# Optimization experiments

Measured on AMD Instinct MI355X. Metric: run time of the kernel, lower is better.

## Reference

```python
import jax, jax.numpy as jnp
import numpy as np
from functools import partial

B, S, T = 32, 64, 64
VS, VT = 32000, 32000
E, H = 256, 512            # embed_dim, encoder hidden per direction
DH = 2 * H                 # decoder hidden (= encoder_hidden_dim)
A = 128                    # attention_dim


def _p(key, shape, scale=0.05):
    return scale * jax.random.normal(key, shape, dtype=jnp.float32)


def setup_inputs() -> dict:
    key = jax.random.key(0)
    ks = jax.random.split(key, 32)
    inp = {
        'src': jax.random.randint(ks[0], (B, S), 0, VS),
        'tgt_input': jax.random.randint(ks[1], (B, T), 0, VT),
        # encoder
        'enc_emb': _p(ks[2], (VS, E)),
        'enc_Wih_f': _p(ks[3], (4 * H, E)), 'enc_Whh_f': _p(ks[4], (4 * H, H)),
        'enc_bih_f': _p(ks[5], (4 * H,)),  'enc_bhh_f': _p(ks[6], (4 * H,)),
        'enc_Wih_b': _p(ks[7], (4 * H, E)), 'enc_Whh_b': _p(ks[8], (4 * H, H)),
        'enc_bih_b': _p(ks[9], (4 * H,)),  'enc_bhh_b': _p(ks[10], (4 * H,)),
        # decoder
        'dec_emb': _p(ks[11], (VT, E)),
        'Wd': _p(ks[12], (A, DH)), 'bd': _p(ks[13], (A,)),
        'We': _p(ks[14], (A, DH)), 'be': _p(ks[15], (A,)),
        'v_att': _p(ks[16], (A,)), 'bv': _p(ks[17], ()),
        'dec_Wih': _p(ks[18], (4 * DH, E + DH)), 'dec_Whh': _p(ks[19], (4 * DH, DH)),
        'dec_bih': _p(ks[20], (4 * DH,)), 'dec_bhh': _p(ks[21], (4 * DH,)),
        'Wo': _p(ks[22], (VT, DH + DH)), 'bo': _p(ks[23], (VT,)),
    }
    return inp


def _lstm_cell(x, h, c, Wih, Whh, b):
    g = x @ Wih.T + h @ Whh.T + b
    i, f, gg, o = jnp.split(g, 4, axis=-1)  # PyTorch gate order: i,f,g,o
    i, f, o = jax.nn.sigmoid(i), jax.nn.sigmoid(f), jax.nn.sigmoid(o)
    c_new = f * c + i * jnp.tanh(gg)
    h_new = o * jnp.tanh(c_new)
    return h_new, c_new


def _lstm_scan(xs, Wih, Whh, b, reverse):
    # xs: [S,B,E] -> outputs [S,B,H] aligned with input positions, final (h,c)
    h0 = jnp.zeros((xs.shape[1], Whh.shape[1]), xs.dtype)
    def step(carry, x):
        h, c = carry
        h, c = _lstm_cell(x, h, c, Wih, Whh, b)
        return (h, c), h
    (hT, cT), hs = jax.lax.scan(step, (h0, h0), xs, reverse=reverse)
    return hs, hT, cT


def _forward(src, tgt_input, enc_emb,
             enc_Wih_f, enc_Whh_f, enc_bih_f, enc_bhh_f,
             enc_Wih_b, enc_Whh_b, enc_bih_b, enc_bhh_b,
             dec_emb, Wd, bd, We, be, v_att, bv,
             dec_Wih, dec_Whh, dec_bih, dec_bhh, Wo, bo):
    # ---- Encoder: bidirectional single-layer LSTM ----
    emb = enc_emb[src]                              # [B,S,E]
    xs = emb.transpose(1, 0, 2)                     # [S,B,E]
    hs_f, hT_f, cT_f = _lstm_scan(xs, enc_Wih_f, enc_Whh_f, enc_bih_f + enc_bhh_f, False)
    hs_b, hT_b, cT_b = _lstm_scan(xs, enc_Wih_b, enc_Whh_b, enc_bih_b + enc_bhh_b, True)
    enc_out = jnp.concatenate([hs_f, hs_b], axis=-1).transpose(1, 0, 2)  # [B,S,2H]
    h = jnp.concatenate([hT_f, hT_b], axis=-1)      # [B,DH]
    c = jnp.concatenate([cT_f, cT_b], axis=-1)

    # ---- Decoder with Bahdanau attention (full teacher forcing) ----
    enc_proj = enc_out @ We.T + be                  # [B,S,A] precomputed
    dec_b = dec_bih + dec_bhh
    tgt_emb = dec_emb[tgt_input].transpose(1, 0, 2)  # [T,B,E]

    def dec_step(carry, emb_t):
        h, c = carry
        dproj = h @ Wd.T + bd                       # [B,A]
        energy = jnp.tanh(dproj[:, None, :] + enc_proj)  # [B,S,A]
        scores = energy @ v_att + bv                # [B,S]
        w = jax.nn.softmax(scores, axis=1)
        ctx = jnp.einsum('bs,bsh->bh', w, enc_out)  # [B,DH]
        x = jnp.concatenate([emb_t, ctx], axis=-1)  # [B,E+DH]
        h_new, c_new = _lstm_cell(x, h, c, dec_Wih, dec_Whh, dec_b)
        logits = jnp.concatenate([h_new, ctx], axis=-1) @ Wo.T + bo  # [B,VT]
        return (h_new, c_new), logits

    _, logits = jax.lax.scan(dec_step, (h, c), tgt_emb)  # [T,B,VT]
    return logits.transpose(1, 0, 2)                     # [B,T,VT]


def reference(src, tgt_input, enc_emb,
              enc_Wih_f, enc_Whh_f, enc_bih_f, enc_bhh_f,
              enc_Wih_b, enc_Whh_b, enc_bih_b, enc_bhh_b,
              dec_emb, Wd, bd, We, be, v_att, bv,
              dec_Wih, dec_Whh, dec_bih, dec_bhh, Wo, bo):
    return _forward(src, tgt_input, enc_emb,
                    enc_Wih_f, enc_Whh_f, enc_bih_f, enc_bhh_f,
                    enc_Wih_b, enc_Whh_b, enc_bih_b, enc_bhh_b,
                    dec_emb, Wd, bd, We, be, v_att, bv,
                    dec_Wih, dec_Whh, dec_bih, dec_bhh, Wo, bo)
```

## Files before the change

### kernel.cpp

```cpp
#include <hip/hip_runtime.h>


using u16 = unsigned short;
using u32 = unsigned int;
using u64 = unsigned long long;
using f32x4 = __attribute__((ext_vector_type(4))) float;
using s16x8 = __attribute__((ext_vector_type(8))) short;
using u16x4 = __attribute__((ext_vector_type(4))) unsigned short;

__device__ __forceinline__ float sigm_(float x) { return 1.0f / (1.0f + expf(-x)); }
__device__ __forceinline__ float tanh_(float x) {
    float e = __expf(fminf(2.0f * x, 30.0f));
    return (e - 1.0f) / (e + 1.0f);
}

__device__ __forceinline__ u16 f2bf(float x) {
    u32 u = __float_as_uint(x);
    u += 0x7fffu + ((u >> 16) & 1u);
    return (u16)(u >> 16);
}
__device__ __forceinline__ u32 pk2(float a, float b) {
    return (u32)f2bf(a) | ((u32)f2bf(b) << 16);
}
__device__ __forceinline__ float bf2f(u16 v) {
    return __uint_as_float((u32)v << 16);
}

__device__ __forceinline__ void ast32(u32* p, u32 v) {
    __hip_atomic_store(p, v, __ATOMIC_RELAXED, __HIP_MEMORY_SCOPE_AGENT);
}

#define MFMA __builtin_amdgcn_mfma_f32_16x16x32_bf16

#define GLL(g, l) __builtin_amdgcn_global_load_lds( \
    (__attribute__((address_space(1))) void*)(g),   \
    (__attribute__((address_space(3))) void*)(l), 16, 0, 0)

__device__ __forceinline__ void gbar(int* cnt, int target) {
    asm volatile("s_waitcnt vmcnt(0) lgkmcnt(0)" ::: "memory");
    __syncthreads();
    if (threadIdx.x == 0) {
        __hip_atomic_fetch_add(cnt, 1, __ATOMIC_RELAXED, __HIP_MEMORY_SCOPE_AGENT);
        while (__hip_atomic_load(cnt, __ATOMIC_RELAXED, __HIP_MEMORY_SCOPE_AGENT) < target)
            __builtin_amdgcn_s_sleep(1);
    }
    __syncthreads();
}

__global__ __launch_bounds__(256) void k_zero(float* __restrict__ p, int n) {
    int i = blockIdx.x * 256 + threadIdx.x;
    if (i < n) p[i] = 0.0f;
}

__global__ __launch_bounds__(256) void k_cast_bf16(const float* __restrict__ in,
                                                   u16* __restrict__ outp, int n8) {
    int idx = blockIdx.x * 256 + threadIdx.x;
    if (idx >= n8) return;
    const f32x4* p = (const f32x4*)in + (size_t)idx * 2;
    f32x4 a = p[0], c = p[1];
    u32* o = (u32*)(outp + (size_t)idx * 8);
    o[0] = pk2(a.x, a.y); o[1] = pk2(a.z, a.w);
    o[2] = pk2(c.x, c.y); o[3] = pk2(c.z, c.w);
}

__global__ __launch_bounds__(256) void k_embed_bf(const int* __restrict__ tok,
                                                  const float* __restrict__ emb,
                                                  u16* __restrict__ outp) {
    int idx = blockIdx.x * 256 + threadIdx.x;
    int r = idx >> 6, e4 = idx & 63;
    int outer = r >> 5, b = r & 31;
    int tk = tok[b * 64 + outer];
    f32x4 v = ((const f32x4*)emb)[(size_t)tk * 64 + e4];
    u32* o = (u32*)(outp + (size_t)r * 256 + (e4 << 2));
    o[0] = pk2(v.x, v.y); o[1] = pk2(v.z, v.w);
}

__global__ __launch_bounds__(256) void k_prep_perm(
    const float* __restrict__ src, u16* __restrict__ dst,
    int J, int K4, int srcStride, int srcOff, int total)
{
    int idx = blockIdx.x * 256 + threadIdx.x;
    if (idx >= total) return;
    int n = idx / K4, kq = (idx - n * K4) << 2;
    int orig = (n & 3) * J + (n >> 2);
    f32x4 v = *(const f32x4*)(src + (size_t)orig * srcStride + srcOff + kq);
    u32* o = (u32*)(dst + (size_t)n * (K4 << 2) + kq);
    o[0] = pk2(v.x, v.y); o[1] = pk2(v.z, v.w);
}

__global__ __launch_bounds__(256) void k_prep_ws(
    const float* __restrict__ W, u16* __restrict__ dst)
{
    int idx = blockIdx.x * 256 + threadIdx.x;
    int n = idx >> 8, kp = idx & 255, k0 = kp << 1;
    int orig = (n & 3) * 512 + (n >> 2);
    const float* s = W + (size_t)orig * 512 + k0;
    int g = n >> 5, r = n & 31;
    int byteoff = (k0 << 1) ^ ((r & 7) << 4);
    *(u32*)((char*)dst + (size_t)g * 32768 + r * 1024 + byteoff) = pk2(s[0], s[1]);
}

__global__ __launch_bounds__(256) void k_prep_w2s(
    const float* __restrict__ Whh, const float* __restrict__ Wih, u16* __restrict__ dst)
{
    int idx = blockIdx.x * 256 + threadIdx.x;
    int n = idx >> 10, kp = idx & 1023, k0 = kp << 1;
    int orig = (n & 3) * 1024 + (n >> 2);
    const float* s = (k0 < 1024) ? (Whh + (size_t)orig * 1024 + k0)
                                 : (Wih + (size_t)orig * 1280 + 256 + (k0 - 1024));
    int g = n >> 5, r = n & 31;
    int byteoff = (k0 << 1) ^ ((r & 7) << 4);
    *(u32*)((char*)dst + (size_t)g * 131072 + r * 4096 + byteoff) = pk2(s[0], s[1]);
}

__global__ __launch_bounds__(256) void k_gemm_bf(
    const u16* __restrict__ A, const u16* __restrict__ B, int K,
    const float* __restrict__ b1, const float* __restrict__ b2, int biasJ,
    float* __restrict__ C, int ldc, int nM, int nN, int remapOut, int swz)
{
    __shared__ __align__(16) u16 As[128 * 32];
    __shared__ __align__(16) u16 Bs[128 * 32];
    int w = blockIdx.x;
    if (swz) { int cpx = (nM * nN) >> 3; w = (w & 7) * cpx + (w >> 3); }
    int bm = (w % nM) * 128, bn = (w / nM) * 128;
    int tid = threadIdx.x, wave = tid >> 6, lane = tid & 63;
    int wm = wave & 1, wn = wave >> 1;
    f32x4 acc[4][4] = {};

    int rA = wave * 32 + (lane >> 2);
    int cb2 = (lane & 3) * 16;
    const char* gA = (const char*)A + ((size_t)(bm + rA) * K) * 2 + cb2;
    const char* gB = (const char*)B + ((size_t)(bn + rA) * K) * 2 + cb2;
    size_t rowskip = (size_t)16 * K * 2;
    char* lA = (char*)As + wave * 2048;
    char* lB = (char*)Bs + wave * 2048;
    const u16* rdA = As + (wm * 64 + (lane & 15)) * 32 + (lane >> 4) * 8;
    const u16* rdB = Bs + (wn * 64 + (lane & 15)) * 32 + (lane >> 4) * 8;

    for (int k0 = 0; k0 < K; k0 += 32) {
        size_t kb = (size_t)k0 * 2;
        GLL(gA + kb, lA); GLL(gA + kb + rowskip, lA + 1024);
        GLL(gB + kb, lB); GLL(gB + kb + rowskip, lB + 1024);
        __syncthreads();
        s16x8 af[4], bfv[4];
#pragma unroll
        for (int m2 = 0; m2 < 4; ++m2) af[m2] = *(const s16x8*)(rdA + m2 * 512);
#pragma unroll
        for (int n2 = 0; n2 < 4; ++n2) bfv[n2] = *(const s16x8*)(rdB + n2 * 512);
#pragma unroll
        for (int m2 = 0; m2 < 4; ++m2)
#pragma unroll
            for (int n2 = 0; n2 < 4; ++n2)
                acc[m2][n2] = MFMA(af[m2], bfv[n2], acc[m2][n2], 0, 0, 0);
        __syncthreads();
    }

    int rbase = bm + wm * 64 + ((lane >> 4) << 2);
    int cbase = bn + wn * 64 + (lane & 15);
#pragma unroll
    for (int n2 = 0; n2 < 4; ++n2) {
        int col = cbase + n2 * 16;
        int bcol = biasJ ? ((col & 3) * biasJ + (col >> 2)) : col;
        float bias = (b1 ? b1[bcol] : 0.0f) + (b2 ? b2[bcol] : 0.0f);
#pragma unroll
        for (int m2 = 0; m2 < 4; ++m2) {
            f32x4 v = acc[m2][n2];
#pragma unroll
            for (int jj = 0; jj < 4; ++jj) {
                int row = rbase + m2 * 16 + jj;
                int orow = remapOut ? ((row & 31) * 64 + (row >> 5)) : row;
                C[(size_t)orow * ldc + col] = v[jj] + bias;
            }
        }
    }
}

__global__ __launch_bounds__(256, 1) void k_enc_persist(
    const u16* __restrict__ Wsf, const u16* __restrict__ Wsb,
    const float* __restrict__ Gfp, const float* __restrict__ Gbp,
    u16* __restrict__ henc,
    float* __restrict__ cfb,
    u16* __restrict__ encbf,
    int* __restrict__ bar)
{
    __shared__ __align__(16) char smem[50176];
    int tid = threadIdx.x, lane = tid & 63, q = tid >> 6;
    int dir = blockIdx.x >> 6, g = blockIdx.x & 63;
    const char* wsrc = (const char*)(dir ? Wsb : Wsf) + (size_t)g * 32768;
#pragma unroll
    for (int it = 0; it < 8; ++it)
        GLL(wsrc + it * 4096 + tid * 16, smem + it * 4096 + tid * 16);
    __syncthreads();

    float* sacc = (float*)(smem + 32768);
    u16* hst = (u16*)(smem + 49664);
    const float* Gp = dir ? Gbp : Gfp;
    float* cB = cfb + dir * 16384;
    int lr = lane & 15, lk = (lane >> 4) << 3;
    int bb = tid & 31, jl = tid >> 5;
    int n0 = g * 32, j = g * 8 + jl;
    int bi = 0;

    for (int s = 0; s < 64; ++s) {
        const u16* hA = henc + (size_t)s * 32768 + dir * 16384;
        s16x8 afr[8];
#pragma unroll
        for (int it = 0; it < 4; ++it) {
            int ke = q * 128 + it * 32 + lk;
            afr[2 * it]     = *(const s16x8*)(hA + lr * 512 + ke);
            afr[2 * it + 1] = *(const s16x8*)(hA + (lr + 16) * 512 + ke);
        }
        f32x4 acc00 = {}, acc01 = {}, acc10 = {}, acc11 = {};
#pragma unroll
        for (int it = 0; it < 4; ++it) {
            int ke = q * 128 + it * 32 + lk;
            int kb = ke << 1;
            s16x8 b0 = *(const s16x8*)(smem + lr * 1024 + (kb ^ ((lr & 7) << 4)));
            int r1 = lr + 16;
            s16x8 b1 = *(const s16x8*)(smem + r1 * 1024 + (kb ^ ((r1 & 7) << 4)));
            acc00 = MFMA(afr[2 * it], b0, acc00, 0, 0, 0);
            acc01 = MFMA(afr[2 * it], b1, acc01, 0, 0, 0);
            acc10 = MFMA(afr[2 * it + 1], b0, acc10, 0, 0, 0);
            acc11 = MFMA(afr[2 * it + 1], b1, acc11, 0, 0, 0);
        }
        int rw = (lane >> 4) << 2;
#pragma unroll
        for (int rr = 0; rr < 4; ++rr) {
            sacc[q * 1056 + (rw + rr) * 33 + lr]        = acc00[rr];
            sacc[q * 1056 + (rw + rr) * 33 + 16 + lr]   = acc01[rr];
            sacc[q * 1056 + (16 + rw + rr) * 33 + lr]      = acc10[rr];
            sacc[q * 1056 + (16 + rw + rr) * 33 + 16 + lr] = acc11[rr];
        }
        __syncthreads();
        {
            int t = dir ? (63 - s) : s;
            int c4 = jl << 2;
            float gi = 0, gf = 0, gg = 0, go2 = 0;
#pragma unroll
            for (int q2 = 0; q2 < 4; ++q2) {
                const float* sp = sacc + q2 * 1056 + bb * 33 + c4;
                gi += sp[0]; gf += sp[1]; gg += sp[2]; go2 += sp[3];
            }
            f32x4 p4 = *(const f32x4*)(Gp + ((size_t)(t * 32 + bb)) * 2048 + n0 + c4);
            gi += p4.x; gf += p4.y; gg += p4.z; go2 += p4.w;
            float* cp = cB + bb * 512 + j;
            float cn = sigm_(gf) * cp[0] + sigm_(gi) * tanhf(gg);
            cp[0] = cn;
            float h = sigm_(go2) * tanhf(cn);
            u16 h16 = f2bf(h);
            encbf[((size_t)(bb * 64 + t)) * 1024 + dir * 512 + j] = h16;
            hst[bb * 8 + jl] = h16;
        }
        __syncthreads();
        if (tid < 128) {
            int bb2 = tid >> 2, p2 = tid & 3;
            u32 wv = (u32)hst[bb2 * 8 + 2 * p2] | ((u32)hst[bb2 * 8 + 2 * p2 + 1] << 16);
            ast32((u32*)(henc + (size_t)(s + 1) * 32768 + dir * 16384) + bb2 * 256 + g * 4 + p2, wv);
        }
        gbar(bar, (++bi) * 128);
    }
}

__global__ __launch_bounds__(256) void k_dec_init(
    const u16* __restrict__ henc, const float* __restrict__ cfb,
    u16* __restrict__ hcarr, float* __restrict__ cd)
{
    int idx = blockIdx.x * 256 + threadIdx.x;
    int b = idx >> 10, j = idx & 1023;
    int dir = (j >> 9), jj = j & 511;
    hcarr[b * 2048 + j] = henc[(size_t)64 * 32768 + dir * 16384 + b * 512 + jj];
    cd[b * 1024 + j] = cfb[dir * 16384 + b * 512 + jj];
}

__global__ __launch_bounds__(256, 1) void k_dec_persist(
    const u16* __restrict__ W2s, const u16* __restrict__ encbf,
    const float* __restrict__ Prep,
    const u16* __restrict__ Wd_bf, const float* __restrict__ bd,
    const float* __restrict__ eproj, const float* __restrict__ v_att,
    const float* __restrict__ bv,
    u16* __restrict__ hcarr, float* __restrict__ cd, u16* __restrict__ Abf,
    int* __restrict__ bar)
{
    __shared__ __align__(16) char smem[148480];
    int blk = blockIdx.x, tid = threadIdx.x, lane = tid & 63, q = tid >> 6;
    bool isgate = blk < 128;
    {
        const char* src = isgate ? ((const char*)W2s + (size_t)blk * 131072)
                                 : ((const char*)encbf + (size_t)(blk - 128) * 131072);
#pragma unroll
        for (int it = 0; it < 32; ++it)
            GLL(src + it * 4096 + tid * 16, smem + it * 4096 + tid * 16);
    }
    __syncthreads();

    float* sacc = (float*)(smem + 131072);
    u16* hst    = (u16*)(smem + 147968);
    float* hsh  = (float*)(smem + 131072);
    float* red  = (float*)(smem + 135168);
    float* dp   = (float*)(smem + 136192);
    float* sc   = (float*)(smem + 136704);

    int lr = lane & 15, lk = (lane >> 4) << 3;
    int bb = tid & 31, jl = tid >> 5;
    int n0 = blk * 32, j = blk * 8 + jl;
    int b = blk - 128;
    int bi = 0;

    for (int t = 0; t < 64; ++t) {
        const u16* hcT = hcarr + (size_t)t * 65536;
        f32x4 acc00 = {}, acc01 = {}, acc10 = {}, acc11 = {};
        f32x4 p4;
        if (isgate) {
            p4 = *(const f32x4*)(Prep + ((size_t)(t * 32 + bb)) * 4096 + n0 + (jl << 2));
            s16x8 afr[16];
#pragma unroll
            for (int it = 0; it < 8; ++it) {
                int ke = q * 256 + it * 32 + lk;
                afr[2 * it]     = *(const s16x8*)(hcT + lr * 2048 + ke);
                afr[2 * it + 1] = *(const s16x8*)(hcT + (lr + 16) * 2048 + ke);
            }
#pragma unroll
            for (int it = 0; it < 8; ++it) {
                int ke = q * 256 + it * 32 + lk;
                int kb = ke << 1;
                s16x8 b0 = *(const s16x8*)(smem + lr * 4096 + (kb ^ ((lr & 7) << 4)));
                int r1 = lr + 16;
                s16x8 b1 = *(const s16x8*)(smem + r1 * 4096 + (kb ^ ((r1 & 7) << 4)));
                acc00 = MFMA(afr[2 * it], b0, acc00, 0, 0, 0);
                acc01 = MFMA(afr[2 * it], b1, acc01, 0, 0, 0);
                acc10 = MFMA(afr[2 * it + 1], b0, acc10, 0, 0, 0);
                acc11 = MFMA(afr[2 * it + 1], b1, acc11, 0, 0, 0);
            }
        } else {
            {
                u16x4 hv = *(const u16x4*)(hcT + b * 2048 + (tid << 2));
                hsh[(tid << 2) + 0] = bf2f(hv.x);
                hsh[(tid << 2) + 1] = bf2f(hv.y);
                hsh[(tid << 2) + 2] = bf2f(hv.z);
                hsh[(tid << 2) + 3] = bf2f(hv.w);
            }
            __syncthreads();
            {
                int a = tid & 127, half = tid >> 7;
                const u16* wr = Wd_bf + ((size_t)a << 10) + (half << 9);
                const float* hh = hsh + (half << 9);
                float s0 = 0, s1 = 0, s2 = 0, s3 = 0;
#pragma unroll 4
                for (int k = 0; k < 512; k += 32) {
                    s16x8 w0 = *(const s16x8*)(wr + k);
                    s16x8 w1 = *(const s16x8*)(wr + k + 8);
                    s16x8 w2 = *(const s16x8*)(wr + k + 16);
                    s16x8 w3 = *(const s16x8*)(wr + k + 24);
#pragma unroll
                    for (int e = 0; e < 8; ++e) {
                        s0 += bf2f((u16)w0[e]) * hh[k + e];
                        s1 += bf2f((u16)w1[e]) * hh[k + 8 + e];
                        s2 += bf2f((u16)w2[e]) * hh[k + 16 + e];
                        s3 += bf2f((u16)w3[e]) * hh[k + 24 + e];
                    }
                }
                red[tid] = (s0 + s1) + (s2 + s3);
            }
            __syncthreads();
            if (tid < 128) dp[tid] = red[tid] + red[tid + 128] + bd[tid];
            __syncthreads();
            {
                int si = tid >> 2, qq = tid & 3;
                const float* ep = eproj + ((size_t)(b * 64 + si)) * 128 + qq * 32;
                float s = 0.0f;
#pragma unroll 8
                for (int a2 = 0; a2 < 32; ++a2)
                    s += v_att[qq * 32 + a2] * tanh_(dp[qq * 32 + a2] + ep[a2]);
                red[tid] = s;
            }
            __syncthreads();
            if (tid < 64) {
                float x = red[tid * 4] + red[tid * 4 + 1] + red[tid * 4 + 2] + red[tid * 4 + 3] + bv[0];
                float mx = x;
#pragma unroll
                for (int off = 32; off; off >>= 1) mx = fmaxf(mx, __shfl_xor(mx, off));
                float e = __expf(x - mx), ss = e;
#pragma unroll
                for (int off = 32; off; off >>= 1) ss += __shfl_xor(ss, off);
                sc[tid] = e / ss;
            }
            __syncthreads();
            {
                const u16* eL = (const u16*)smem;
                int c0i = tid << 2;
                float c0 = 0, c1 = 0, c2 = 0, c3 = 0;
                for (int s2 = 0; s2 < 64; ++s2) {
                    float wgt = sc[s2];
                    u16x4 rp = *(const u16x4*)(eL + s2 * 1024 + c0i);
                    c0 += wgt * bf2f(rp.x); c1 += wgt * bf2f(rp.y);
                    c2 += wgt * bf2f(rp.z); c3 += wgt * bf2f(rp.w);
                }
                u32 w0 = pk2(c0, c1), w1 = pk2(c2, c3);
                u32* hw = (u32*)hcT + b * 1024 + 512 + (tid << 1);
                ast32(hw, w0); ast32(hw + 1, w1);
                u32* aw = (u32*)(Abf + ((size_t)(t * 32 + b)) * 2048 + 1024 + c0i);
                aw[0] = w0; aw[1] = w1;
            }
        }
        gbar(bar, (++bi) * 160);
        if (isgate) {
            s16x8 afr[16];
#pragma unroll
            for (int it = 0; it < 8; ++it) {
                int ke = 1024 + q * 256 + it * 32 + lk;
                afr[2 * it]     = *(const s16x8*)(hcT + lr * 2048 + ke);
                afr[2 * it + 1] = *(const s16x8*)(hcT + (lr + 16) * 2048 + ke);
            }
#pragma unroll
            for (int it = 0; it < 8; ++it) {
                int ke = 1024 + q * 256 + it * 32 + lk;
                int kb = ke << 1;
                s16x8 b0 = *(const s16x8*)(smem + lr * 4096 + (kb ^ ((lr & 7) << 4)));
                int r1 = lr + 16;
                s16x8 b1 = *(const s16x8*)(smem + r1 * 4096 + (kb ^ ((r1 & 7) << 4)));
                acc00 = MFMA(afr[2 * it], b0, acc00, 0, 0, 0);
                acc01 = MFMA(afr[2 * it], b1, acc01, 0, 0, 0);
                acc10 = MFMA(afr[2 * it + 1], b0, acc10, 0, 0, 0);
                acc11 = MFMA(afr[2 * it + 1], b1, acc11, 0, 0, 0);
            }
            int rw = (lane >> 4) << 2;
#pragma unroll
            for (int rr = 0; rr < 4; ++rr) {
                sacc[q * 1056 + (rw + rr) * 33 + lr]        = acc00[rr];
                sacc[q * 1056 + (rw + rr) * 33 + 16 + lr]   = acc01[rr];
                sacc[q * 1056 + (16 + rw + rr) * 33 + lr]      = acc10[rr];
                sacc[q * 1056 + (16 + rw + rr) * 33 + 16 + lr] = acc11[rr];
            }
            __syncthreads();
            {
                int c4 = jl << 2;
                float gi = 0, gf = 0, gg = 0, go2 = 0;
#pragma unroll
                for (int q2 = 0; q2 < 4; ++q2) {
                    const float* sp = sacc + q2 * 1056 + bb * 33 + c4;
                    gi += sp[0]; gf += sp[1]; gg += sp[2]; go2 += sp[3];
                }
                gi += p4.x; gf += p4.y; gg += p4.z; go2 += p4.w;
                int ci = bb * 1024 + j;
                float cn = sigm_(gf) * cd[ci] + sigm_(gi) * tanhf(gg);
                cd[ci] = cn;
                float h = sigm_(go2) * tanhf(cn);
                u16 h16 = f2bf(h);
                Abf[((size_t)(t * 32 + bb)) * 2048 + j] = h16;
                hst[bb * 8 + jl] = h16;
            }
            __syncthreads();
            if (tid < 128) {
                int bb2 = tid >> 2, p2 = tid & 3;
                u32 wv = (u32)hst[bb2 * 8 + 2 * p2] | ((u32)hst[bb2 * 8 + 2 * p2 + 1] << 16);
                ast32((u32*)(hcarr + (size_t)(t + 1) * 65536) + bb2 * 1024 + blk * 4 + p2, wv);
            }
        }
        gbar(bar, (++bi) * 160);
    }
}

extern "C" void kernel_launch(void* const* d_in, const int* in_sizes, int n_in,
                              void* d_out, int out_size, void* d_ws, size_t ws_size,
                              hipStream_t stream)
{
    (void)in_sizes; (void)n_in; (void)out_size; (void)ws_size;
    const int*   src     = (const int*)d_in[0];
    const int*   tgt     = (const int*)d_in[1];
    const float* enc_emb = (const float*)d_in[2];
    const float* eWih_f  = (const float*)d_in[3];
    const float* eWhh_f  = (const float*)d_in[4];
    const float* ebih_f  = (const float*)d_in[5];
    const float* ebhh_f  = (const float*)d_in[6];
    const float* eWih_b  = (const float*)d_in[7];
    const float* eWhh_b  = (const float*)d_in[8];
    const float* ebih_b  = (const float*)d_in[9];
    const float* ebhh_b  = (const float*)d_in[10];
    const float* dec_emb = (const float*)d_in[11];
    const float* Wd      = (const float*)d_in[12];
    const float* bd      = (const float*)d_in[13];
    const float* We      = (const float*)d_in[14];
    const float* be      = (const float*)d_in[15];
    const float* v_att   = (const float*)d_in[16];
    const float* bv      = (const float*)d_in[17];
    const float* dWih    = (const float*)d_in[18];
    const float* dWhh    = (const float*)d_in[19];
    const float* dbih    = (const float*)d_in[20];
    const float* dbhh    = (const float*)d_in[21];
    const float* Wo      = (const float*)d_in[22];
    const float* bo      = (const float*)d_in[23];
    float* out = (float*)d_out;

    char* wp = (char*)d_ws;
    auto alloc = [&](size_t nbytes) -> void* {
        void* p = (void*)wp;
        wp += (nbytes + 255) & ~(size_t)255;
        return p;
    };
    u16*   Xe_bf = (u16*)alloc(2048u * 256 * 2);
    u16*   Ed_bf = (u16*)alloc(2048u * 256 * 2);
    float* Gf_p  = (float*)alloc(2048u * 2048 * 4);
    float* Gb_p  = (float*)alloc(2048u * 2048 * 4);
    float* Pre_p = (float*)alloc(2048u * 4096 * 4);
    float* zr    = (float*)alloc(131584u);
    float* cfb   = zr;
    int*   cnts  = (int*)((char*)zr + 131072);
    u16*   henc  = (u16*)alloc(65u * 32768 * 2);
    u16*   hcarr = (u16*)alloc(65u * 65536 * 2);
    u16*   encbf = (u16*)alloc(2048u * 1024 * 2);
    float* eproj = (float*)alloc(2048u * 128 * 4);
    float* cd    = (float*)alloc(32768u * 4);
    u16*   Abf   = (u16*)alloc(2048u * 2048 * 2);
    u16*   Wbf   = (u16*)alloc(32000u * 2048 * 2);
    u16*   W2s   = (u16*)alloc(4096u * 2048 * 2);
    u16*   Wsf   = (u16*)alloc(2048u * 512 * 2);
    u16*   Wsb   = (u16*)alloc(2048u * 512 * 2);
    u16*   Wembf = (u16*)alloc(2048u * 256 * 2);
    u16*   Wembb = (u16*)alloc(2048u * 256 * 2);
    u16*   Wembd = (u16*)alloc(4096u * 256 * 2);
    u16*   We_bf = (u16*)alloc(128u * 1024 * 2);
    u16*   Wd_bf = (u16*)alloc(128u * 1024 * 2);

    k_zero<<<129, 256, 0, stream>>>(zr, 32896);
    k_zero<<<64, 256, 0, stream>>>((float*)henc, 16384);

    k_cast_bf16<<<32000, 256, 0, stream>>>(Wo, Wbf, 8192000);
    k_cast_bf16<<<64, 256, 0, stream>>>(We, We_bf, 16384);
    k_cast_bf16<<<64, 256, 0, stream>>>(Wd, Wd_bf, 16384);
    k_prep_perm<<<512, 256, 0, stream>>>(eWih_f, Wembf, 512, 64, 256, 0, 131072);
    k_prep_perm<<<512, 256, 0, stream>>>(eWih_b, Wembb, 512, 64, 256, 0, 131072);
    k_prep_perm<<<1024, 256, 0, stream>>>(dWih, Wembd, 1024, 64, 1280, 0, 262144);
    k_prep_ws<<<2048, 256, 0, stream>>>(eWhh_f, Wsf);
    k_prep_ws<<<2048, 256, 0, stream>>>(eWhh_b, Wsb);
    k_prep_w2s<<<16384, 256, 0, stream>>>(dWhh, dWih, W2s);

    k_embed_bf<<<512, 256, 0, stream>>>(src, enc_emb, Xe_bf);
    k_embed_bf<<<512, 256, 0, stream>>>(tgt, dec_emb, Ed_bf);

    k_gemm_bf<<<256, 256, 0, stream>>>(Xe_bf, Wembf, 256, ebih_f, ebhh_f, 512,
                                       Gf_p, 2048, 16, 16, 0, 1);
    k_gemm_bf<<<256, 256, 0, stream>>>(Xe_bf, Wembb, 256, ebih_b, ebhh_b, 512,
                                       Gb_p, 2048, 16, 16, 0, 1);
    k_gemm_bf<<<512, 256, 0, stream>>>(Ed_bf, Wembd, 256, dbih, dbhh, 1024,
                                       Pre_p, 4096, 16, 32, 0, 1);

    k_enc_persist<<<128, 256, 0, stream>>>(Wsf, Wsb, Gf_p, Gb_p, henc, cfb, encbf, cnts);

    k_gemm_bf<<<16, 256, 0, stream>>>(encbf, We_bf, 1024, be, nullptr, 0,
                                      eproj, 128, 16, 1, 0, 1);
    k_dec_init<<<128, 256, 0, stream>>>(henc, cfb, hcarr, cd);

    k_dec_persist<<<160, 256, 0, stream>>>(W2s, encbf, Pre_p, Wd_bf, bd, eproj,
                                           v_att, bv, hcarr, cd, Abf, cnts + 64);

    k_gemm_bf<<<4000, 256, 0, stream>>>(Abf, Wbf, 2048, bo, nullptr, 0,
                                        out, 32000, 16, 250, 1, 1);
}
```

Baseline: 2.375 ms.

## Replace global barriers with per-step sharded counters and split producer/consumer flags

```diff
diff --git a/kernel.cpp b/kernel.cpp
--- a/kernel.cpp
+++ b/kernel.cpp
@@ -36,15 +36,24 @@
     (__attribute__((address_space(1))) void*)(g),   \
     (__attribute__((address_space(3))) void*)(l), 16, 0, 0)
 
-__device__ __forceinline__ void gbar(int* cnt, int target) {
+__device__ __forceinline__ void poll8(const int* go8) {
+    if (threadIdx.x < 8) {
+        const int* p = go8 + threadIdx.x * 16;
+        while (__hip_atomic_load(p, __ATOMIC_RELAXED, __HIP_MEMORY_SCOPE_AGENT) == 0)
+            __builtin_amdgcn_s_sleep(1);
+    }
+    __syncthreads();
+    asm volatile("" ::: "memory");
+}
+__device__ __forceinline__ void arrive8(int* cnt8, int* go8, int line, int perline) {
     asm volatile("s_waitcnt vmcnt(0) lgkmcnt(0)" ::: "memory");
     __syncthreads();
     if (threadIdx.x == 0) {
-        __hip_atomic_fetch_add(cnt, 1, __ATOMIC_RELAXED, __HIP_MEMORY_SCOPE_AGENT);
-        while (__hip_atomic_load(cnt, __ATOMIC_RELAXED, __HIP_MEMORY_SCOPE_AGENT) < target)
-            __builtin_amdgcn_s_sleep(1);
-    }
-    __syncthreads();
+        int old = __hip_atomic_fetch_add(cnt8 + line * 16, 1, __ATOMIC_RELAXED,
+                                         __HIP_MEMORY_SCOPE_AGENT);
+        if (old == perline - 1)
+            __hip_atomic_store(go8 + line * 16, 1, __ATOMIC_RELAXED, __HIP_MEMORY_SCOPE_AGENT);
+    }
 }
 
 __global__ __launch_bounds__(256) void k_zero(float* __restrict__ p, int n) {
@@ -181,7 +190,7 @@
     u16* __restrict__ henc,
     float* __restrict__ cfb,
     u16* __restrict__ encbf,
-    int* __restrict__ bar)
+    int* __restrict__ cnt8, int* __restrict__ go8)
 {
     __shared__ __align__(16) char smem[50176];
     int tid = threadIdx.x, lane = tid & 63, q = tid >> 6;
@@ -199,9 +208,11 @@
     int lr = lane & 15, lk = (lane >> 4) << 3;
     int bb = tid & 31, jl = tid >> 5;
     int n0 = g * 32, j = g * 8 + jl;
-    int bi = 0;
 
     for (int s = 0; s < 64; ++s) {
+        if (s) poll8(go8 + s * 128);
+        int t = dir ? (63 - s) : s;
+        f32x4 p4 = *(const f32x4*)(Gp + ((size_t)(t * 32 + bb)) * 2048 + n0 + (jl << 2));
         const u16* hA = henc + (size_t)s * 32768 + dir * 16384;
         s16x8 afr[8];
 #pragma unroll
@@ -233,7 +244,6 @@
         }
         __syncthreads();
         {
-            int t = dir ? (63 - s) : s;
             int c4 = jl << 2;
             float gi = 0, gf = 0, gg = 0, go2 = 0;
 #pragma unroll
@@ -241,7 +251,6 @@
                 const float* sp = sacc + q2 * 1056 + bb * 33 + c4;
                 gi += sp[0]; gf += sp[1]; gg += sp[2]; go2 += sp[3];
             }
-            f32x4 p4 = *(const f32x4*)(Gp + ((size_t)(t * 32 + bb)) * 2048 + n0 + c4);
             gi += p4.x; gf += p4.y; gg += p4.z; go2 += p4.w;
             float* cp = cB + bb * 512 + j;
             float cn = sigm_(gf) * cp[0] + sigm_(gi) * tanhf(gg);
@@ -257,7 +266,7 @@
             u32 wv = (u32)hst[bb2 * 8 + 2 * p2] | ((u32)hst[bb2 * 8 + 2 * p2 + 1] << 16);
             ast32((u32*)(henc + (size_t)(s + 1) * 32768 + dir * 16384) + bb2 * 256 + g * 4 + p2, wv);
         }
-        gbar(bar, (++bi) * 128);
+        arrive8(cnt8 + (s + 1) * 128, go8 + (s + 1) * 128, blockIdx.x & 7, 16);
     }
 }
 
@@ -279,7 +288,8 @@
     const float* __restrict__ eproj, const float* __restrict__ v_att,
     const float* __restrict__ bv,
     u16* __restrict__ hcarr, float* __restrict__ cd, u16* __restrict__ Abf,
-    int* __restrict__ bar)
+    int* __restrict__ hCnt8, int* __restrict__ goH8,
+    int* __restrict__ ctxCnt8, int* __restrict__ goCtx8)
 {
     __shared__ __align__(16) char smem[148480];
     int blk = blockIdx.x, tid = threadIdx.x, lane = tid & 63, q = tid >> 6;
@@ -304,14 +314,12 @@
     int bb = tid & 31, jl = tid >> 5;
     int n0 = blk * 32, j = blk * 8 + jl;
     int b = blk - 128;
-    int bi = 0;
 
     for (int t = 0; t < 64; ++t) {
+        if (t) poll8(goH8 + t * 128);
         const u16* hcT = hcarr + (size_t)t * 65536;
-        f32x4 acc00 = {}, acc01 = {}, acc10 = {}, acc11 = {};
-        f32x4 p4;
         if (isgate) {
-            p4 = *(const f32x4*)(Prep + ((size_t)(t * 32 + bb)) * 4096 + n0 + (jl << 2));
+            f32x4 p4 = *(const f32x4*)(Prep + ((size_t)(t * 32 + bb)) * 4096 + n0 + (jl << 2));
             s16x8 afr[16];
 #pragma unroll
             for (int it = 0; it < 8; ++it) {
@@ -319,6 +327,7 @@
                 afr[2 * it]     = *(const s16x8*)(hcT + lr * 2048 + ke);
                 afr[2 * it + 1] = *(const s16x8*)(hcT + (lr + 16) * 2048 + ke);
             }
+            f32x4 acc00 = {}, acc01 = {}, acc10 = {}, acc11 = {};
 #pragma unroll
             for (int it = 0; it < 8; ++it) {
                 int ke = q * 256 + it * 32 + lk;
@@ -331,80 +340,7 @@
                 acc10 = MFMA(afr[2 * it + 1], b0, acc10, 0, 0, 0);
                 acc11 = MFMA(afr[2 * it + 1], b1, acc11, 0, 0, 0);
             }
-        } else {
-            {
-                u16x4 hv = *(const u16x4*)(hcT + b * 2048 + (tid << 2));
-                hsh[(tid << 2) + 0] = bf2f(hv.x);
-                hsh[(tid << 2) + 1] = bf2f(hv.y);
-                hsh[(tid << 2) + 2] = bf2f(hv.z);
-                hsh[(tid << 2) + 3] = bf2f(hv.w);
-            }
-            __syncthreads();
-            {
-                int a = tid & 127, half = tid >> 7;
-                const u16* wr = Wd_bf + ((size_t)a << 10) + (half << 9);
-                const float* hh = hsh + (half << 9);
-                float s0 = 0, s1 = 0, s2 = 0, s3 = 0;
-#pragma unroll 4
-                for (int k = 0; k < 512; k += 32) {
-                    s16x8 w0 = *(const s16x8*)(wr + k);
-                    s16x8 w1 = *(const s16x8*)(wr + k + 8);
-                    s16x8 w2 = *(const s16x8*)(wr + k + 16);
-                    s16x8 w3 = *(const s16x8*)(wr + k + 24);
-#pragma unroll
-                    for (int e = 0; e < 8; ++e) {
-                        s0 += bf2f((u16)w0[e]) * hh[k + e];
-                        s1 += bf2f((u16)w1[e]) * hh[k + 8 + e];
-                        s2 += bf2f((u16)w2[e]) * hh[k + 16 + e];
-                        s3 += bf2f((u16)w3[e]) * hh[k + 24 + e];
-                    }
-                }
-                red[tid] = (s0 + s1) + (s2 + s3);
-            }
-            __syncthreads();
-            if (tid < 128) dp[tid] = red[tid] + red[tid + 128] + bd[tid];
-            __syncthreads();
-            {
-                int si = tid >> 2, qq = tid & 3;
-                const float* ep = eproj + ((size_t)(b * 64 + si)) * 128 + qq * 32;
-                float s = 0.0f;
-#pragma unroll 8
-                for (int a2 = 0; a2 < 32; ++a2)
-                    s += v_att[qq * 32 + a2] * tanh_(dp[qq * 32 + a2] + ep[a2]);
-                red[tid] = s;
-            }
-            __syncthreads();
-            if (tid < 64) {
-                float x = red[tid * 4] + red[tid * 4 + 1] + red[tid * 4 + 2] + red[tid * 4 + 3] + bv[0];
-                float mx = x;
-#pragma unroll
-                for (int off = 32; off; off >>= 1) mx = fmaxf(mx, __shfl_xor(mx, off));
-                float e = __expf(x - mx), ss = e;
-#pragma unroll
-                for (int off = 32; off; off >>= 1) ss += __shfl_xor(ss, off);
-                sc[tid] = e / ss;
-            }
-            __syncthreads();
-            {
-                const u16* eL = (const u16*)smem;
-                int c0i = tid << 2;
-                float c0 = 0, c1 = 0, c2 = 0, c3 = 0;
-                for (int s2 = 0; s2 < 64; ++s2) {
-                    float wgt = sc[s2];
-                    u16x4 rp = *(const u16x4*)(eL + s2 * 1024 + c0i);
-                    c0 += wgt * bf2f(rp.x); c1 += wgt * bf2f(rp.y);
-                    c2 += wgt * bf2f(rp.z); c3 += wgt * bf2f(rp.w);
-                }
-                u32 w0 = pk2(c0, c1), w1 = pk2(c2, c3);
-                u32* hw = (u32*)hcT + b * 1024 + 512 + (tid << 1);
-                ast32(hw, w0); ast32(hw + 1, w1);
-                u32* aw = (u32*)(Abf + ((size_t)(t * 32 + b)) * 2048 + 1024 + c0i);
-                aw[0] = w0; aw[1] = w1;
-            }
-        }
-        gbar(bar, (++bi) * 160);
-        if (isgate) {
-            s16x8 afr[16];
+            poll8(goCtx8 + t * 128);
 #pragma unroll
             for (int it = 0; it < 8; ++it) {
                 int ke = 1024 + q * 256 + it * 32 + lk;
@@ -455,8 +391,82 @@
                 u32 wv = (u32)hst[bb2 * 8 + 2 * p2] | ((u32)hst[bb2 * 8 + 2 * p2 + 1] << 16);
                 ast32((u32*)(hcarr + (size_t)(t + 1) * 65536) + bb2 * 1024 + blk * 4 + p2, wv);
             }
-        }
-        gbar(bar, (++bi) * 160);
+            arrive8(hCnt8 + (t + 1) * 128, goH8 + (t + 1) * 128, blk & 7, 16);
+        } else {
+            {
+                u16x4 hv = *(const u16x4*)(hcT + b * 2048 + (tid << 2));
+                hsh[(tid << 2) + 0] = bf2f(hv.x);
+                hsh[(tid << 2) + 1] = bf2f(hv.y);
+                hsh[(tid << 2) + 2] = bf2f(hv.z);
+                hsh[(tid << 2) + 3] = bf2f(hv.w);
+            }
+            __syncthreads();
+            {
+                int a = tid & 127, half = tid >> 7;
+                const u16* wr = Wd_bf + ((size_t)a << 10) + (half << 9);
+                const float* hh = hsh + (half << 9);
+                float s0 = 0, s1 = 0, s2 = 0, s3 = 0;
+#pragma unroll 4
+                for (int k = 0; k < 512; k += 32) {
+                    s16x8 w0 = *(const s16x8*)(wr + k);
+                    s16x8 w1 = *(const s16x8*)(wr + k + 8);
+                    s16x8 w2 = *(const s16x8*)(wr + k + 16);
+                    s16x8 w3 = *(const s16x8*)(wr + k + 24);
+#pragma unroll
+                    for (int e = 0; e < 8; ++e) {
+                        s0 += bf2f((u16)w0[e]) * hh[k + e];
+                        s1 += bf2f((u16)w1[e]) * hh[k + 8 + e];
+                        s2 += bf2f((u16)w2[e]) * hh[k + 16 + e];
+                        s3 += bf2f((u16)w3[e]) * hh[k + 24 + e];
+                    }
+                }
+                red[tid] = (s0 + s1) + (s2 + s3);
+            }
+            __syncthreads();
+            if (tid < 128) dp[tid] = red[tid] + red[tid + 128] + bd[tid];
+            __syncthreads();
+            {
+                int si = tid >> 2, qq = tid & 3;
+                const float* ep = eproj + ((size_t)(b * 64 + si)) * 128 + qq * 32;
+                float s = 0.0f;
+#pragma unroll 8
+                for (int a2 = 0; a2 < 32; ++a2)
+                    s += v_att[qq * 32 + a2] * tanh_(dp[qq * 32 + a2] + ep[a2]);
+                red[tid] = s;
+            }
+            __syncthreads();
+            if (tid < 64) {
+                float x = red[tid * 4] + red[tid * 4 + 1] + red[tid * 4 + 2] + red[tid * 4 + 3] + bv[0];
+                float mx = x;
+#pragma unroll
+                for (int off = 32; off; off >>= 1) mx = fmaxf(mx, __shfl_xor(mx, off));
+                float e = __expf(x - mx), ss = e;
+#pragma unroll
+                for (int off = 32; off; off >>= 1) ss += __shfl_xor(ss, off);
+                sc[tid] = e / ss;
+            }
+            __syncthreads();
+            u32 cw0, cw1;
+            {
+                const u16* eL = (const u16*)smem;
+                int c0i = tid << 2;
+                float c0 = 0, c1 = 0, c2 = 0, c3 = 0;
+                for (int s2 = 0; s2 < 64; ++s2) {
+                    float wgt = sc[s2];
+                    u16x4 rp = *(const u16x4*)(eL + s2 * 1024 + c0i);
+                    c0 += wgt * bf2f(rp.x); c1 += wgt * bf2f(rp.y);
+                    c2 += wgt * bf2f(rp.z); c3 += wgt * bf2f(rp.w);
+                }
+                cw0 = pk2(c0, c1); cw1 = pk2(c2, c3);
+                u32* hw = (u32*)hcT + b * 1024 + 512 + (tid << 1);
+                ast32(hw, cw0); ast32(hw + 1, cw1);
+            }
+            arrive8(ctxCnt8 + t * 128, goCtx8 + t * 128, blk & 7, 4);
+            {
+                u32* aw = (u32*)(Abf + ((size_t)(t * 32 + b)) * 2048 + 1024 + (tid << 2));
+                aw[0] = cw0; aw[1] = cw1;
+            }
+        }
     }
 }
 
@@ -502,9 +512,15 @@
     float* Gf_p  = (float*)alloc(2048u * 2048 * 4);
     float* Gb_p  = (float*)alloc(2048u * 2048 * 4);
     float* Pre_p = (float*)alloc(2048u * 4096 * 4);
-    float* zr    = (float*)alloc(131584u);
+    float* zr    = (float*)alloc(329728u);
     float* cfb   = zr;
-    int*   cnts  = (int*)((char*)zr + 131072);
+    char*  sy    = (char*)zr + 131072;
+    int*   cntE8 = (int*)(sy);
+    int*   goE8  = (int*)(sy + 33280);
+    int*   hCnt8 = (int*)(sy + 66560);
+    int*   goH8  = (int*)(sy + 99840);
+    int*   ctxC8 = (int*)(sy + 133120);
+    int*   goX8  = (int*)(sy + 165888);
     u16*   henc  = (u16*)alloc(65u * 32768 * 2);
     u16*   hcarr = (u16*)alloc(65u * 65536 * 2);
     u16*   encbf = (u16*)alloc(2048u * 1024 * 2);
@@ -521,7 +537,7 @@
     u16*   We_bf = (u16*)alloc(128u * 1024 * 2);
     u16*   Wd_bf = (u16*)alloc(128u * 1024 * 2);
 
-    k_zero<<<129, 256, 0, stream>>>(zr, 32896);
+    k_zero<<<322, 256, 0, stream>>>(zr, 82432);
     k_zero<<<64, 256, 0, stream>>>((float*)henc, 16384);
 
     k_cast_bf16<<<32000, 256, 0, stream>>>(Wo, Wbf, 8192000);
@@ -544,14 +560,16 @@
     k_gemm_bf<<<512, 256, 0, stream>>>(Ed_bf, Wembd, 256, dbih, dbhh, 1024,
                                        Pre_p, 4096, 16, 32, 0, 1);
 
-    k_enc_persist<<<128, 256, 0, stream>>>(Wsf, Wsb, Gf_p, Gb_p, henc, cfb, encbf, cnts);
+    k_enc_persist<<<128, 256, 0, stream>>>(Wsf, Wsb, Gf_p, Gb_p, henc, cfb, encbf,
+                                           cntE8, goE8);
 
     k_gemm_bf<<<16, 256, 0, stream>>>(encbf, We_bf, 1024, be, nullptr, 0,
                                       eproj, 128, 16, 1, 0, 1);
     k_dec_init<<<128, 256, 0, stream>>>(henc, cfb, hcarr, cd);
 
     k_dec_persist<<<160, 256, 0, stream>>>(W2s, encbf, Pre_p, Wd_bf, bd, eproj,
-                                           v_att, bv, hcarr, cd, Abf, cnts + 64);
+                                           v_att, bv, hcarr, cd, Abf,
+                                           hCnt8, goH8, ctxC8, goX8);
 
     k_gemm_bf<<<4000, 256, 0, stream>>>(Abf, Wbf, 2048, bo, nullptr, 0,
                                         out, 32000, 16, 250, 1, 1);
```

Result: faster. 2.015 ms (-15.1%).
